# Kernel tuning notes

Hardware: AMD Instinct MI355X
Metric: run time of the kernel (lower is better)

The kernel has to match this reference:

```python
import jax, jax.numpy as jnp
import numpy as np

B, N, R, S, G = 16, 10000, 10, 1000, 4
DIN, DH = 32, 64
DBLK = DIN + DH  # block input dim = input_dim + rnn_units
BIAS_W = jnp.array([0.1, 0.1, 0.1, 1.0], dtype=jnp.float32)


def _block(h, A, rs, W, a1w, a1b, a2w, a2b):
    # h: [B,N,din], A: [G,R,S,S] (shared across batch), rs: [B,N,2]
    Bb, Nn, din = h.shape
    hr = h.reshape(Bb, R, S, din)
    deg = jnp.clip(A.sum(-1), 1e-5) ** -0.5                     # [G,R,S]
    eye = jnp.eye(S, dtype=A.dtype)
    An = deg[..., :, None] * (A + eye) * deg[..., None, :]      # sym-normalized A+I
    hw = jnp.einsum('brsd,gde->gbrse', hr, W)                   # [G,B,R,S,DH]
    outs = jax.nn.relu(jnp.einsum('grst,gbrte->gbrse', An, hw)).reshape(G, Bb, Nn, DH)
    H = jnp.moveaxis(outs, 0, -2).reshape(Bb, Nn, G * DH)       # cat over graphs
    z = jax.nn.relu(jnp.concatenate([H, rs], -1) @ a1w + a1b)
    alpha = jax.nn.softmax(z @ a2w + a2b, axis=-1)              # [B,N,G]
    bias = (rs[:, :, 1] > 0.5).astype(h.dtype)[..., None] * BIAS_W
    alpha = alpha * (1.0 + bias)
    alpha = alpha / alpha.sum(-1, keepdims=True)
    return jnp.einsum('bng,gbne->bne', alpha, outs)


def setup_inputs() -> dict:
    key = jax.random.key(0)
    ks = jax.random.split(key, 16)
    inp = {
        'x_t': jax.random.normal(ks[0], (B, N, DIN), jnp.float32),
        'h_prev': jax.random.normal(ks[1], (B, N, DH), jnp.float32),
        'A': jax.random.uniform(ks[2], (G, R, S, S), jnp.float32),
        'resid_stats': jax.random.uniform(ks[3], (B, N, 2), jnp.float32),
    }
    i = 4
    for tag in ('u', 'r', 'c'):
        inp['W_' + tag] = jax.random.normal(ks[i], (G, DBLK, DH), jnp.float32) * 0.05; i += 1
        inp['a1w_' + tag] = jax.random.normal(ks[i], (G * DH + 2, DH), jnp.float32) * 0.05; i += 1
        inp['a1b_' + tag] = jnp.zeros((DH,), jnp.float32)
        inp['a2w_' + tag] = jax.random.normal(ks[i], (DH, G), jnp.float32) * 0.05; i += 1
        inp['a2b_' + tag] = jnp.zeros((G,), jnp.float32)
    return inp


def reference(x_t, h_prev, A, resid_stats,
              W_u, a1w_u, a1b_u, a2w_u, a2b_u,
              W_r, a1w_r, a1b_r, a2w_r, a2b_r,
              W_c, a1w_c, a1b_c, a2w_c, a2b_c):
    inp = jnp.concatenate([x_t, h_prev], -1)
    U = _block(inp, A, resid_stats, W_u, a1w_u, a1b_u, a2w_u, a2b_u)
    Rg = _block(inp, A, resid_stats, W_r, a1w_r, a1b_r, a2w_r, a2b_r)
    cand = jnp.concatenate([x_t, Rg * h_prev], -1)
    Ht = _block(cand, A, resid_stats, W_c, a1w_c, a1b_c, a2w_c, a2b_c)
    u = jax.nn.sigmoid(U)
    return u * jnp.tanh(Ht) + (1.0 - u) * h_prev
```

## Files before the change

### kernel.cpp

```cpp
#include <hip/hip_runtime.h>

typedef unsigned short u16;
typedef __attribute__((ext_vector_type(8))) short bfrag8;
typedef __attribute__((ext_vector_type(4))) float fvec4;
typedef __attribute__((ext_vector_type(4))) unsigned short usvec4;

#define Bc   16
#define Nn   10000
#define Rr   10
#define Ss   1000
#define Gg   4
#define SP   1024
#define NPAD 10048

__device__ __forceinline__ float bf2f(u16 u) {
  union { unsigned int i; float f; } x; x.i = ((unsigned int)u) << 16; return x.f;
}
__device__ __forceinline__ u16 f2bf(float f) {
  unsigned int x = __float_as_uint(f);
  unsigned int r = x + 0x7FFFu + ((x >> 16) & 1u);
  return (u16)(r >> 16);
}

__global__ __launch_bounds__(256) void prep_weights_kernel(
    const float* __restrict__ Wu, const float* __restrict__ Wr, const float* __restrict__ Wc,
    const float* __restrict__ a1u, const float* __restrict__ a1r, const float* __restrict__ a1c,
    u16* __restrict__ Wt, u16* __restrict__ a1wb)
{
  int idx = blockIdx.x * 256 + threadIdx.x;
  if (idx < 73728) {
    int p = idx / 24576, rem = idx % 24576;
    int g = rem / 6144, r2 = rem % 6144;
    int e = r2 / 96, dd = r2 % 96;
    const float* W = (p == 0) ? Wu : (p == 1) ? Wr : Wc;
    Wt[idx] = f2bf(W[(g * 96 + dd) * 64 + e]);
  } else if (idx < 73728 + 49536) {
    int j = idx - 73728;
    int p = j / 16512, k = j % 16512;
    const float* s = (p == 0) ? a1u : (p == 1) ? a1r : a1c;
    a1wb[j] = f2bf(s[k]);
  }
}

__global__ __launch_bounds__(256) void rowsum_kernel(const float* __restrict__ A,
                                                     float* __restrict__ dis)
{
  int wid = threadIdx.x >> 6, lane = threadIdx.x & 63;
  int row = blockIdx.x * 4 + wid;
  const float* ap = A + (size_t)row * 1000;
  float s = 0.f;
  for (int i = lane; i < 250; i += 64) {
    float4 v = *(const float4*)(ap + i * 4);
    s += (v.x + v.y) + (v.z + v.w);
  }
  #pragma unroll
  for (int off = 32; off >= 1; off >>= 1) s += __shfl_xor(s, off);
  if (lane == 0) dis[row] = rsqrtf(fmaxf(s, 1e-5f));
}

__global__ __launch_bounds__(256) void build_an_kernel(const float* __restrict__ A,
                                                       const float* __restrict__ dis,
                                                       u16* __restrict__ An)
{
  int rowid = blockIdx.x;
  int gr = rowid / 1000, s = rowid % 1000;
  float ds = dis[rowid];
  const float* ap = A + (size_t)rowid * 1000;
  u16* anp = An + (size_t)rowid * SP;
  int t4 = threadIdx.x * 4;
  if (t4 < 1000) {
    float4 a4 = *(const float4*)(ap + t4);
    float4 d4 = *(const float4*)(dis + gr * 1000 + t4);
    float v0 = ds * d4.x * (a4.x + ((t4 + 0) == s ? 1.f : 0.f));
    float v1 = ds * d4.y * (a4.y + ((t4 + 1) == s ? 1.f : 0.f));
    float v2 = ds * d4.z * (a4.z + ((t4 + 2) == s ? 1.f : 0.f));
    float v3 = ds * d4.w * (a4.w + ((t4 + 3) == s ? 1.f : 0.f));
    usvec4 o = {f2bf(v0), f2bf(v1), f2bf(v2), f2bf(v3)};
    *(usvec4*)(anp + t4) = o;
  } else {
    usvec4 o = {0, 0, 0, 0};
    *(usvec4*)(anp + t4) = o;
  }
}

__global__ __launch_bounds__(256) void prep_inpT_kernel(const float* __restrict__ x_t,
                                                        const float* __restrict__ h_prev,
                                                        u16* __restrict__ inpT)
{
  int b = blockIdx.y, n0 = blockIdx.x * 64;
  __shared__ float t[64][97];
  for (int idx = threadIdx.x; idx < 2048; idx += 256) {
    int ni = idx >> 5, d = idx & 31;
    int n = n0 + ni;
    t[ni][d] = (n < Nn) ? x_t[(size_t)(b * Nn + n) * 32 + d] : 0.f;
  }
  for (int idx = threadIdx.x; idx < 4096; idx += 256) {
    int ni = idx >> 6, d = idx & 63;
    int n = n0 + ni;
    t[ni][32 + d] = (n < Nn) ? h_prev[(size_t)(b * Nn + n) * 64 + d] : 0.f;
  }
  __syncthreads();
  for (int idx = threadIdx.x; idx < 6144; idx += 256) {
    int d = idx >> 6, ni = idx & 63;
    inpT[(size_t)b * (96 * NPAD) + (size_t)d * NPAD + n0 + ni] = f2bf(t[ni][d]);
  }
}

template <int NPROJ>
__global__ __launch_bounds__(256) void gemm_pass_kernel(
    const u16* __restrict__ An,
    const u16* __restrict__ inpT,
    const u16* __restrict__ Wt,
    u16* __restrict__ outs0, u16* __restrict__ outs1)
{
  constexpr int BT_OFF = 128 * 40;
  __shared__ __align__(16) u16 lds_main[12288];

  const int tid = threadIdx.x;
  const int lane = tid & 63, wid = tid >> 6;
  const int mt = blockIdx.x, b = blockIdx.y, gr = blockIdx.z;
  const int g = gr / Rr, r = gr % Rr;
  const int m0 = mt * 128;
  const int wrow0 = wid * 32;
  const int lr = lane & 15, lk = (lane >> 4) << 3;

  const u16* Ap = An + (size_t)gr * (Ss * SP);
  const u16* Bp = inpT + (size_t)b * (96 * NPAD) + r * Ss;

  fvec4 acc[2][6];
  #pragma unroll
  for (int i = 0; i < 2; ++i)
    #pragma unroll
    for (int j = 0; j < 6; ++j) acc[i][j] = (fvec4){0.f, 0.f, 0.f, 0.f};

  #pragma unroll 1
  for (int kk = 0; kk < SP; kk += 32) {
    __syncthreads();
    #pragma unroll
    for (int s2 = 0; s2 < 2; ++s2) {
      int seg = tid + (s2 << 8);
      int row = seg >> 2, kl = (seg & 3) << 3;
      int srow = m0 + row;
      bfrag8 v = (bfrag8){0, 0, 0, 0, 0, 0, 0, 0};
      if (srow < Ss) v = *(const bfrag8*)(Ap + (size_t)srow * SP + kk + kl);
      *(bfrag8*)&lds_main[row * 40 + kl] = v;
    }
    {
      int d = tid >> 2, tl = (tid & 3) << 3;
      *(bfrag8*)&lds_main[BT_OFF + d * 40 + tl] = *(const bfrag8*)(Bp + (size_t)d * NPAD + kk + tl);
      if (tid < 128) {
        int seg = 256 + tid;
        int d2 = seg >> 2, t2 = (seg & 3) << 3;
        *(bfrag8*)&lds_main[BT_OFF + d2 * 40 + t2] = *(const bfrag8*)(Bp + (size_t)d2 * NPAD + kk + t2);
      }
    }
    __syncthreads();
    bfrag8 af0 = *(const bfrag8*)&lds_main[(wrow0 + lr) * 40 + lk];
    bfrag8 af1 = *(const bfrag8*)&lds_main[(wrow0 + 16 + lr) * 40 + lk];
    #pragma unroll
    for (int nf = 0; nf < 6; ++nf) {
      bfrag8 bfr = *(const bfrag8*)&lds_main[BT_OFF + (nf * 16 + lr) * 40 + lk];
      acc[0][nf] = __builtin_amdgcn_mfma_f32_16x16x32_bf16(af0, bfr, acc[0][nf], 0, 0, 0);
      acc[1][nf] = __builtin_amdgcn_mfma_f32_16x16x32_bf16(af1, bfr, acc[1][nf], 0, 0, 0);
    }
  }

  __syncthreads();
  #pragma unroll
  for (int mf = 0; mf < 2; ++mf)
    #pragma unroll
    for (int nf = 0; nf < 6; ++nf)
      #pragma unroll
      for (int j = 0; j < 4; ++j) {
        int row = wrow0 + mf * 16 + ((lane >> 4) << 2) + j;
        lds_main[row * 96 + nf * 16 + lr] = f2bf(acc[mf][nf][j]);
      }
  __syncthreads();

  const int obase = ((g * Bc + b) * Nn + r * Ss) * 64;
  #pragma unroll
  for (int p = 0; p < NPROJ; ++p) {
    const u16* Wg = Wt + (size_t)(p * Gg + g) * 6144;
    fvec4 acc2[2][4];
    #pragma unroll
    for (int i = 0; i < 2; ++i)
      #pragma unroll
      for (int j = 0; j < 4; ++j) acc2[i][j] = (fvec4){0.f, 0.f, 0.f, 0.f};
    #pragma unroll
    for (int dk = 0; dk < 96; dk += 32) {
      bfrag8 x0 = *(const bfrag8*)&lds_main[(wrow0 + lr) * 96 + dk + lk];
      bfrag8 x1 = *(const bfrag8*)&lds_main[(wrow0 + 16 + lr) * 96 + dk + lk];
      #pragma unroll
      for (int ef = 0; ef < 4; ++ef) {
        bfrag8 wv = *(const bfrag8*)&Wg[(ef * 16 + lr) * 96 + dk + lk];
        acc2[0][ef] = __builtin_amdgcn_mfma_f32_16x16x32_bf16(x0, wv, acc2[0][ef], 0, 0, 0);
        acc2[1][ef] = __builtin_amdgcn_mfma_f32_16x16x32_bf16(x1, wv, acc2[1][ef], 0, 0, 0);
      }
    }
    u16* op = (p == 0) ? outs0 : outs1;
    #pragma unroll
    for (int mf = 0; mf < 2; ++mf)
      #pragma unroll
      for (int ef = 0; ef < 4; ++ef)
        #pragma unroll
        for (int j = 0; j < 4; ++j) {
          int srow = m0 + wrow0 + mf * 16 + ((lane >> 4) << 2) + j;
          if (srow < Ss) {
            float v = fmaxf(acc2[mf][ef][j], 0.f);
            op[obase + srow * 64 + ef * 16 + lr] = f2bf(v);
          }
        }
  }
}

template <int MODE>
__global__ __launch_bounds__(256) void attn_kernel(
    const u16* __restrict__ outs,
    const float* __restrict__ rs,
    const u16* __restrict__ a1wb,
    const float* __restrict__ a1b, const float* __restrict__ a2w, const float* __restrict__ a2b,
    const float* __restrict__ h_prev, const float* __restrict__ u_sig_in,
    float* __restrict__ usig_out, u16* __restrict__ candh_out, float* __restrict__ out_final)
{
  __shared__ __align__(16) u16 a1wT[16384];
  __shared__ __align__(16) u16 Hs[16384];
  __shared__ __align__(16) float alpha_s[256];

  const int tid = threadIdx.x, lane = tid & 63, w = tid >> 6;
  const int lr16 = lane & 15, hi4 = lane >> 4;
  const int lk = hi4 << 3;
  const int w16 = w * 16;

  {
    int e = tid & 63, kb = (tid >> 6) * 64;
    for (int i = 0; i < 64; ++i) {
      int k = kb + i;
      a1wT[(e * 256 + k) ^ ((e & 7) << 3)] = a1wb[k * 64 + e];
    }
  }

  float a1b_v[4], w256v[4], w257v[4], a2w_l[16], a2b_v[4];
  #pragma unroll
  for (int ef = 0; ef < 4; ++ef) {
    int e = ef * 16 + lr16;
    a1b_v[ef] = a1b[e];
    w256v[ef] = bf2f(a1wb[256 * 64 + e]);
    w257v[ef] = bf2f(a1wb[257 * 64 + e]);
    #pragma unroll
    for (int g = 0; g < 4; ++g) a2w_l[ef * 4 + g] = a2w[e * 4 + g];
  }
  #pragma unroll
  for (int g = 0; g < 4; ++g) a2b_v[g] = a2b[g];

  for (int it = 0; it < 5; ++it) {
    const int row0 = (blockIdx.x * 5 + it) * 64;
    __syncthreads();
    #pragma unroll
    for (int j = 0; j < 8; ++j) {
      int c = tid + j * 256;
      int g = c >> 9, rem = c & 511, ri = rem >> 3, e8 = rem & 7;
      bfrag8 v = *(const bfrag8*)&outs[((size_t)g * (Bc * Nn) + row0 + ri) * 64 + e8 * 8];
      *(bfrag8*)&Hs[(ri * 256 + g * 64 + e8 * 8) ^ ((ri & 7) << 3)] = v;
    }
    __syncthreads();

    fvec4 zacc[4];
    #pragma unroll
    for (int ef = 0; ef < 4; ++ef) zacc[ef] = (fvec4){0.f, 0.f, 0.f, 0.f};
    #pragma unroll
    for (int ks = 0; ks < 8; ++ks) {
      bfrag8 af = *(const bfrag8*)&Hs[((w16 + lr16) * 256 + ks * 32 + lk) ^ ((lr16 & 7) << 3)];
      #pragma unroll
      for (int ef = 0; ef < 4; ++ef) {
        bfrag8 bf = *(const bfrag8*)&a1wT[((ef * 16 + lr16) * 256 + ks * 32 + lk) ^ ((lr16 & 7) << 3)];
        zacc[ef] = __builtin_amdgcn_mfma_f32_16x16x32_bf16(af, bf, zacc[ef], 0, 0, 0);
      }
    }

    float r0[4], r1[4];
    #pragma unroll
    for (int j = 0; j < 4; ++j) {
      int rrow = row0 + w16 + hi4 * 4 + j;
      float2 rv = *(const float2*)(rs + (size_t)rrow * 2);
      r0[j] = rv.x; r1[j] = rv.y;
    }
    float pj[16];
    #pragma unroll
    for (int i = 0; i < 16; ++i) pj[i] = 0.f;
    #pragma unroll
    for (int ef = 0; ef < 4; ++ef)
      #pragma unroll
      for (int j = 0; j < 4; ++j) {
        float zv = zacc[ef][j] + a1b_v[ef] + r0[j] * w256v[ef] + r1[j] * w257v[ef];
        zv = fmaxf(zv, 0.f);
        #pragma unroll
        for (int g = 0; g < 4; ++g) pj[j * 4 + g] = fmaf(zv, a2w_l[ef * 4 + g], pj[j * 4 + g]);
      }
    #pragma unroll
    for (int off = 1; off <= 8; off <<= 1)
      #pragma unroll
      for (int i = 0; i < 16; ++i) pj[i] += __shfl_xor(pj[i], off);

    #pragma unroll
    for (int j = 0; j < 4; ++j) {
      float p0 = pj[j * 4 + 0] + a2b_v[0], p1 = pj[j * 4 + 1] + a2b_v[1];
      float p2 = pj[j * 4 + 2] + a2b_v[2], p3 = pj[j * 4 + 3] + a2b_v[3];
      float m = fmaxf(fmaxf(p0, p1), fmaxf(p2, p3));
      float e0 = __expf(p0 - m), e1 = __expf(p1 - m), e2 = __expf(p2 - m), e3 = __expf(p3 - m);
      if (r1[j] > 0.5f) { e0 *= 1.1f; e1 *= 1.1f; e2 *= 1.1f; e3 *= 2.0f; }
      float inv = 1.f / (e0 + e1 + e2 + e3);
      if (lr16 < 4) {
        float esel = (lr16 == 0) ? e0 : (lr16 == 1) ? e1 : (lr16 == 2) ? e2 : e3;
        alpha_s[(w16 + hi4 * 4 + j) * 4 + lr16] = esel * inv;
      }
    }

    #pragma unroll 1
    for (int rr = 0; rr < 16; ++rr) {
      int lrow = w16 + rr;
      float4 av = *(const float4*)&alpha_s[lrow * 4];
      int sw = (lrow & 7) << 3, base = lrow * 256;
      float cmb = av.x * bf2f(Hs[(base + lane) ^ sw])
                + av.y * bf2f(Hs[(base + 64 + lane) ^ sw])
                + av.z * bf2f(Hs[(base + 128 + lane) ^ sw])
                + av.w * bf2f(Hs[(base + 192 + lane) ^ sw]);
      size_t gi = (size_t)(row0 + lrow) * 64 + lane;
      if (MODE == 0) {
        usig_out[gi] = 1.f / (1.f + __expf(-cmb));
      } else if (MODE == 1) {
        candh_out[gi] = f2bf(cmb * h_prev[gi]);
      } else {
        float u = u_sig_in[gi], hp = h_prev[gi];
        out_final[gi] = u * tanhf(cmb) + (1.f - u) * hp;
      }
    }
  }
}

__global__ __launch_bounds__(256) void transpose_cand_kernel(const u16* __restrict__ candh,
                                                             u16* __restrict__ inpT)
{
  int b = blockIdx.y, n0 = blockIdx.x * 64;
  __shared__ float t[64][65];
  for (int idx = threadIdx.x; idx < 4096; idx += 256) {
    int ni = idx >> 6, e = idx & 63;
    int n = n0 + ni;
    t[ni][e] = (n < Nn) ? bf2f(candh[(size_t)(b * Nn + n) * 64 + e]) : 0.f;
  }
  __syncthreads();
  for (int idx = threadIdx.x; idx < 4096; idx += 256) {
    int e = idx >> 6, ni = idx & 63;
    inpT[(size_t)b * (96 * NPAD) + (size_t)(32 + e) * NPAD + n0 + ni] = f2bf(t[ni][e]);
  }
}

extern "C" void kernel_launch(void* const* d_in, const int* in_sizes, int n_in,
                              void* d_out, int out_size, void* d_ws, size_t ws_size,
                              hipStream_t stream) {
  (void)in_sizes; (void)n_in; (void)out_size; (void)ws_size;
  const float* x_t    = (const float*)d_in[0];
  const float* h_prev = (const float*)d_in[1];
  const float* A      = (const float*)d_in[2];
  const float* rs     = (const float*)d_in[3];
  const float* W_u    = (const float*)d_in[4];
  const float* a1w_u  = (const float*)d_in[5];
  const float* a1b_u  = (const float*)d_in[6];
  const float* a2w_u  = (const float*)d_in[7];
  const float* a2b_u  = (const float*)d_in[8];
  const float* W_r    = (const float*)d_in[9];
  const float* a1w_r  = (const float*)d_in[10];
  const float* a1b_r  = (const float*)d_in[11];
  const float* a2w_r  = (const float*)d_in[12];
  const float* a2b_r  = (const float*)d_in[13];
  const float* W_c    = (const float*)d_in[14];
  const float* a1w_c  = (const float*)d_in[15];
  const float* a1b_c  = (const float*)d_in[16];
  const float* a2w_c  = (const float*)d_in[17];
  const float* a2b_c  = (const float*)d_in[18];
  float* out = (float*)d_out;

  char* ws = (char*)d_ws;
  const size_t AN_OFF    = 0;
  const size_t DIS_OFF   = 81920000;
  const size_t INPT_OFF  = 82080000;
  const size_t OUTSU_OFF = 112947456;
  const size_t OUTSR_OFF = 194867456;
  const size_t USIG_OFF  = 276787456;
  const size_t CANDH_OFF = 317747456;
  const size_t WT_OFF    = 338227456;
  const size_t A1WB_OFF  = 338374912;

  u16* An    = (u16*)(ws + AN_OFF);
  float* dis = (float*)(ws + DIS_OFF);
  u16* inpT  = (u16*)(ws + INPT_OFF);
  u16* outsU = (u16*)(ws + OUTSU_OFF);
  u16* outsR = (u16*)(ws + OUTSR_OFF);
  u16* outsC = outsU;
  float* usig = (float*)(ws + USIG_OFF);
  u16* candh = (u16*)(ws + CANDH_OFF);
  u16* Wt    = (u16*)(ws + WT_OFF);
  u16* a1wb  = (u16*)(ws + A1WB_OFF);

  prep_weights_kernel<<<482, 256, 0, stream>>>(W_u, W_r, W_c, a1w_u, a1w_r, a1w_c, Wt, a1wb);
  rowsum_kernel<<<10000, 256, 0, stream>>>(A, dis);
  build_an_kernel<<<40000, 256, 0, stream>>>(A, dis, An);
  prep_inpT_kernel<<<dim3(157, 16), 256, 0, stream>>>(x_t, h_prev, inpT);

  gemm_pass_kernel<2><<<dim3(8, 16, 40), 256, 0, stream>>>(An, inpT, Wt, outsU, outsR);

  attn_kernel<0><<<500, 256, 0, stream>>>(outsU, rs, a1wb, a1b_u, a2w_u, a2b_u,
                                          nullptr, nullptr, usig, nullptr, nullptr);
  attn_kernel<1><<<500, 256, 0, stream>>>(outsR, rs, a1wb + 16512, a1b_r, a2w_r, a2b_r,
                                          h_prev, nullptr, nullptr, candh, nullptr);
  transpose_cand_kernel<<<dim3(157, 16), 256, 0, stream>>>(candh, inpT);

  gemm_pass_kernel<1><<<dim3(8, 16, 40), 256, 0, stream>>>(An, inpT, Wt + 2 * 24576, outsC, nullptr);

  attn_kernel<2><<<500, 256, 0, stream>>>(outsC, rs, a1wb + 2 * 16512, a1b_c, a2w_c, a2b_c,
                                          h_prev, usig, nullptr, nullptr, out);
}
```

Before: 1.156 ms.

## Restructure GRU graph GEMMs with direct-to-LDS loads and reordered candidate projection

Replaces the A-hat x input GEMM with a version that stages tiles via global_load_lds into XOR-swizzled LDS with 64-wide K steps and a 2x2 wave layout. The candidate block now projects through W first (cand_proj_kernel) and then multiplies by An with a wider N tile. That removes the 96-dim input GEMM and the separate transpose kernel. The attention kernels take a pre-transposed a1w from global memory instead of rebuilding it in LDS, run one tile per block across more blocks, and store usig as bf16. An is padded to 1024 rows so loads need no bounds checks. The costs are extra workspace layout changes and somewhat more bf16 rounding.

```diff
diff --git a/kernel.cpp b/kernel.cpp
--- a/kernel.cpp
+++ b/kernel.cpp
@@ -11,6 +11,7 @@
 #define Ss   1000
 #define Gg   4
 #define SP   1024
+#define MP   1024
 #define NPAD 10048
 
 __device__ __forceinline__ float bf2f(u16 u) {
@@ -22,10 +23,28 @@
   return (u16)(r >> 16);
 }
 
+__device__ __forceinline__ void glds16(const u16* gsrc, u16* ldst) {
+  __builtin_amdgcn_global_load_lds((const __attribute__((address_space(1))) unsigned int*)gsrc,
+                                   (__attribute__((address_space(3))) unsigned int*)ldst, 16, 0, 0);
+}
+
+__device__ __forceinline__ void stage_tile(const u16* gsrc, size_t rstride, int nloads,
+                                           u16* ldsbase, int wid, int lane) {
+  int rsub = lane >> 3;
+  int kb8 = ((lane & 7) ^ rsub) << 3;
+  for (int i = wid; i < nloads; i += 4)
+    glds16(gsrc + (size_t)(8 * i + rsub) * rstride + kb8, ldsbase + i * 512);
+}
+
+__device__ __forceinline__ bfrag8 ldsw(const u16* base, int row, int kbyte) {
+  int off = row * 128 + (kbyte ^ ((row & 7) << 4));
+  return *(const bfrag8*)((const char*)base + off);
+}
+
 __global__ __launch_bounds__(256) void prep_weights_kernel(
     const float* __restrict__ Wu, const float* __restrict__ Wr, const float* __restrict__ Wc,
     const float* __restrict__ a1u, const float* __restrict__ a1r, const float* __restrict__ a1c,
-    u16* __restrict__ Wt, u16* __restrict__ a1wb)
+    u16* __restrict__ Wt, u16* __restrict__ a1wb, u16* __restrict__ a1wT)
 {
   int idx = blockIdx.x * 256 + threadIdx.x;
   if (idx < 73728) {
@@ -39,6 +58,12 @@
     int p = j / 16512, k = j % 16512;
     const float* s = (p == 0) ? a1u : (p == 1) ? a1r : a1c;
     a1wb[j] = f2bf(s[k]);
+  } else if (idx < 73728 + 49536 + 49152) {
+    int j = idx - 123264;
+    int p = j / 16384, rem = j % 16384;
+    int e = rem / 256, k = rem % 256;
+    const float* s = (p == 0) ? a1u : (p == 1) ? a1r : a1c;
+    a1wT[j] = f2bf(s[k * 64 + e]);
   }
 }
 
@@ -62,30 +87,31 @@
                                                        const float* __restrict__ dis,
                                                        u16* __restrict__ An)
 {
-  int rowid = blockIdx.x;
-  int gr = rowid / 1000, s = rowid % 1000;
+  int gr = blockIdx.x >> 10, s = blockIdx.x & 1023;
+  u16* anp = An + (size_t)blockIdx.x * 1024;
+  int t4 = threadIdx.x * 4;
+  if (s >= Ss || t4 >= 1000) {
+    usvec4 z = {0, 0, 0, 0};
+    *(usvec4*)(anp + t4) = z;
+    return;
+  }
+  int rowid = gr * 1000 + s;
   float ds = dis[rowid];
   const float* ap = A + (size_t)rowid * 1000;
-  u16* anp = An + (size_t)rowid * SP;
-  int t4 = threadIdx.x * 4;
-  if (t4 < 1000) {
-    float4 a4 = *(const float4*)(ap + t4);
-    float4 d4 = *(const float4*)(dis + gr * 1000 + t4);
-    float v0 = ds * d4.x * (a4.x + ((t4 + 0) == s ? 1.f : 0.f));
-    float v1 = ds * d4.y * (a4.y + ((t4 + 1) == s ? 1.f : 0.f));
-    float v2 = ds * d4.z * (a4.z + ((t4 + 2) == s ? 1.f : 0.f));
-    float v3 = ds * d4.w * (a4.w + ((t4 + 3) == s ? 1.f : 0.f));
-    usvec4 o = {f2bf(v0), f2bf(v1), f2bf(v2), f2bf(v3)};
-    *(usvec4*)(anp + t4) = o;
-  } else {
-    usvec4 o = {0, 0, 0, 0};
-    *(usvec4*)(anp + t4) = o;
-  }
+  float4 a4 = *(const float4*)(ap + t4);
+  float4 d4 = *(const float4*)(dis + gr * 1000 + t4);
+  float v0 = ds * d4.x * (a4.x + ((t4 + 0) == s ? 1.f : 0.f));
+  float v1 = ds * d4.y * (a4.y + ((t4 + 1) == s ? 1.f : 0.f));
+  float v2 = ds * d4.z * (a4.z + ((t4 + 2) == s ? 1.f : 0.f));
+  float v3 = ds * d4.w * (a4.w + ((t4 + 3) == s ? 1.f : 0.f));
+  usvec4 o = {f2bf(v0), f2bf(v1), f2bf(v2), f2bf(v3)};
+  *(usvec4*)(anp + t4) = o;
 }
 
 __global__ __launch_bounds__(256) void prep_inpT_kernel(const float* __restrict__ x_t,
                                                         const float* __restrict__ h_prev,
-                                                        u16* __restrict__ inpT)
+                                                        u16* __restrict__ inpT,
+                                                        u16* __restrict__ candb)
 {
   int b = blockIdx.y, n0 = blockIdx.x * 64;
   __shared__ float t[64][97];
@@ -104,82 +130,77 @@
     int d = idx >> 6, ni = idx & 63;
     inpT[(size_t)b * (96 * NPAD) + (size_t)d * NPAD + n0 + ni] = f2bf(t[ni][d]);
   }
-}
-
-template <int NPROJ>
-__global__ __launch_bounds__(256) void gemm_pass_kernel(
+  for (int idx = threadIdx.x; idx < 2048; idx += 256) {
+    int ni = idx >> 5, d = idx & 31;
+    int n = n0 + ni;
+    if (n < Nn) candb[((size_t)b * Nn + n) * 96 + d] = f2bf(t[ni][d]);
+  }
+}
+
+__global__ __launch_bounds__(256) void gemm_uv_kernel(
     const u16* __restrict__ An,
     const u16* __restrict__ inpT,
     const u16* __restrict__ Wt,
     u16* __restrict__ outs0, u16* __restrict__ outs1)
 {
-  constexpr int BT_OFF = 128 * 40;
-  __shared__ __align__(16) u16 lds_main[12288];
-
-  const int tid = threadIdx.x;
-  const int lane = tid & 63, wid = tid >> 6;
+  __shared__ __align__(1024) u16 lds[14336];
+
+  const int tid = threadIdx.x, lane = tid & 63, wid = tid >> 6;
   const int mt = blockIdx.x, b = blockIdx.y, gr = blockIdx.z;
   const int g = gr / Rr, r = gr % Rr;
   const int m0 = mt * 128;
-  const int wrow0 = wid * 32;
-  const int lr = lane & 15, lk = (lane >> 4) << 3;
-
-  const u16* Ap = An + (size_t)gr * (Ss * SP);
+  const int wrow0 = (wid >> 1) * 64, wcol0 = (wid & 1) * 48;
+  const int lr = lane & 15, hi = lane >> 4;
+  const int kbhi = hi * 16;
+
+  const u16* Ap = An + (size_t)gr * (MP * SP) + (size_t)m0 * SP;
   const u16* Bp = inpT + (size_t)b * (96 * NPAD) + r * Ss;
 
-  fvec4 acc[2][6];
-  #pragma unroll
-  for (int i = 0; i < 2; ++i)
-    #pragma unroll
-    for (int j = 0; j < 6; ++j) acc[i][j] = (fvec4){0.f, 0.f, 0.f, 0.f};
+  fvec4 acc[4][3];
+  #pragma unroll
+  for (int i = 0; i < 4; ++i)
+    #pragma unroll
+    for (int j = 0; j < 3; ++j) acc[i][j] = (fvec4){0.f, 0.f, 0.f, 0.f};
 
   #pragma unroll 1
-  for (int kk = 0; kk < SP; kk += 32) {
+  for (int kt = 0; kt < 16; ++kt) {
+    const int kk = kt * 64;
     __syncthreads();
-    #pragma unroll
-    for (int s2 = 0; s2 < 2; ++s2) {
-      int seg = tid + (s2 << 8);
-      int row = seg >> 2, kl = (seg & 3) << 3;
-      int srow = m0 + row;
-      bfrag8 v = (bfrag8){0, 0, 0, 0, 0, 0, 0, 0};
-      if (srow < Ss) v = *(const bfrag8*)(Ap + (size_t)srow * SP + kk + kl);
-      *(bfrag8*)&lds_main[row * 40 + kl] = v;
-    }
-    {
-      int d = tid >> 2, tl = (tid & 3) << 3;
-      *(bfrag8*)&lds_main[BT_OFF + d * 40 + tl] = *(const bfrag8*)(Bp + (size_t)d * NPAD + kk + tl);
-      if (tid < 128) {
-        int seg = 256 + tid;
-        int d2 = seg >> 2, t2 = (seg & 3) << 3;
-        *(bfrag8*)&lds_main[BT_OFF + d2 * 40 + t2] = *(const bfrag8*)(Bp + (size_t)d2 * NPAD + kk + t2);
-      }
-    }
+    stage_tile(Ap + kk, SP, 16, lds, wid, lane);
+    stage_tile(Bp + kk, NPAD, 12, lds + 8192, wid, lane);
     __syncthreads();
-    bfrag8 af0 = *(const bfrag8*)&lds_main[(wrow0 + lr) * 40 + lk];
-    bfrag8 af1 = *(const bfrag8*)&lds_main[(wrow0 + 16 + lr) * 40 + lk];
-    #pragma unroll
-    for (int nf = 0; nf < 6; ++nf) {
-      bfrag8 bfr = *(const bfrag8*)&lds_main[BT_OFF + (nf * 16 + lr) * 40 + lk];
-      acc[0][nf] = __builtin_amdgcn_mfma_f32_16x16x32_bf16(af0, bfr, acc[0][nf], 0, 0, 0);
-      acc[1][nf] = __builtin_amdgcn_mfma_f32_16x16x32_bf16(af1, bfr, acc[1][nf], 0, 0, 0);
+    #pragma unroll
+    for (int ks = 0; ks < 2; ++ks) {
+      bfrag8 a[4], bb[3];
+      #pragma unroll
+      for (int mfi = 0; mfi < 4; ++mfi) a[mfi] = ldsw(lds, wrow0 + mfi * 16 + lr, ks * 64 + kbhi);
+      #pragma unroll
+      for (int nfi = 0; nfi < 3; ++nfi) bb[nfi] = ldsw(lds + 8192, wcol0 + nfi * 16 + lr, ks * 64 + kbhi);
+      #pragma unroll
+      for (int mfi = 0; mfi < 4; ++mfi)
+        #pragma unroll
+        for (int nfi = 0; nfi < 3; ++nfi)
+          acc[mfi][nfi] = __builtin_amdgcn_mfma_f32_16x16x32_bf16(a[mfi], bb[nfi], acc[mfi][nfi], 0, 0, 0);
     }
   }
 
   __syncthreads();
   #pragma unroll
-  for (int mf = 0; mf < 2; ++mf)
-    #pragma unroll
-    for (int nf = 0; nf < 6; ++nf)
+  for (int mfi = 0; mfi < 4; ++mfi)
+    #pragma unroll
+    for (int nfi = 0; nfi < 3; ++nfi)
       #pragma unroll
       for (int j = 0; j < 4; ++j) {
-        int row = wrow0 + mf * 16 + ((lane >> 4) << 2) + j;
-        lds_main[row * 96 + nf * 16 + lr] = f2bf(acc[mf][nf][j]);
+        int row = wrow0 + mfi * 16 + hi * 4 + j;
+        int col = wcol0 + nfi * 16 + lr;
+        lds[row * 104 + col] = f2bf(acc[mfi][nfi][j]);
       }
   __syncthreads();
 
+  const int s2r0 = wid * 32;
   const int obase = ((g * Bc + b) * Nn + r * Ss) * 64;
   #pragma unroll
-  for (int p = 0; p < NPROJ; ++p) {
+  for (int p = 0; p < 2; ++p) {
     const u16* Wg = Wt + (size_t)(p * Gg + g) * 6144;
     fvec4 acc2[2][4];
     #pragma unroll
@@ -187,12 +208,12 @@
       #pragma unroll
       for (int j = 0; j < 4; ++j) acc2[i][j] = (fvec4){0.f, 0.f, 0.f, 0.f};
     #pragma unroll
-    for (int dk = 0; dk < 96; dk += 32) {
-      bfrag8 x0 = *(const bfrag8*)&lds_main[(wrow0 + lr) * 96 + dk + lk];
-      bfrag8 x1 = *(const bfrag8*)&lds_main[(wrow0 + 16 + lr) * 96 + dk + lk];
+    for (int dk = 0; dk < 3; ++dk) {
+      bfrag8 x0 = *(const bfrag8*)&lds[(s2r0 + lr) * 104 + dk * 32 + kbhi / 2];
+      bfrag8 x1 = *(const bfrag8*)&lds[(s2r0 + 16 + lr) * 104 + dk * 32 + kbhi / 2];
       #pragma unroll
       for (int ef = 0; ef < 4; ++ef) {
-        bfrag8 wv = *(const bfrag8*)&Wg[(ef * 16 + lr) * 96 + dk + lk];
+        bfrag8 wv = *(const bfrag8*)&Wg[(ef * 16 + lr) * 96 + dk * 32 + kbhi / 2];
         acc2[0][ef] = __builtin_amdgcn_mfma_f32_16x16x32_bf16(x0, wv, acc2[0][ef], 0, 0, 0);
         acc2[1][ef] = __builtin_amdgcn_mfma_f32_16x16x32_bf16(x1, wv, acc2[1][ef], 0, 0, 0);
       }
@@ -204,7 +225,7 @@
       for (int ef = 0; ef < 4; ++ef)
         #pragma unroll
         for (int j = 0; j < 4; ++j) {
-          int srow = m0 + wrow0 + mf * 16 + ((lane >> 4) << 2) + j;
+          int srow = m0 + s2r0 + mf * 16 + hi * 4 + j;
           if (srow < Ss) {
             float v = fmaxf(acc2[mf][ef][j], 0.f);
             op[obase + srow * 64 + ef * 16 + lr] = f2bf(v);
@@ -213,16 +234,128 @@
   }
 }
 
+__global__ __launch_bounds__(256) void cand_proj_kernel(const u16* __restrict__ candb,
+                                                        const u16* __restrict__ Wt,
+                                                        u16* __restrict__ hwcT)
+{
+  __shared__ __align__(16) u16 lds[16384];
+  const int tid = threadIdx.x, lane = tid & 63, g = tid >> 6;
+  const int lr = lane & 15, hi = lane >> 4;
+  const int b = blockIdx.y, n0 = blockIdx.x * 64;
+  const u16* WcT = Wt + (size_t)(2 * Gg + g) * 6144;
+
+  fvec4 acc[4][4];
+  #pragma unroll
+  for (int i = 0; i < 4; ++i)
+    #pragma unroll
+    for (int j = 0; j < 4; ++j) acc[i][j] = (fvec4){0.f, 0.f, 0.f, 0.f};
+
+  #pragma unroll
+  for (int ks = 0; ks < 3; ++ks) {
+    bfrag8 a[4], w[4];
+    #pragma unroll
+    for (int mfi = 0; mfi < 4; ++mfi)
+      a[mfi] = *(const bfrag8*)&candb[((size_t)b * Nn + n0 + mfi * 16 + lr) * 96 + ks * 32 + hi * 8];
+    #pragma unroll
+    for (int nfi = 0; nfi < 4; ++nfi)
+      w[nfi] = *(const bfrag8*)&WcT[(nfi * 16 + lr) * 96 + ks * 32 + hi * 8];
+    #pragma unroll
+    for (int mfi = 0; mfi < 4; ++mfi)
+      #pragma unroll
+      for (int nfi = 0; nfi < 4; ++nfi)
+        acc[mfi][nfi] = __builtin_amdgcn_mfma_f32_16x16x32_bf16(a[mfi], w[nfi], acc[mfi][nfi], 0, 0, 0);
+  }
+
+  #pragma unroll
+  for (int mfi = 0; mfi < 4; ++mfi)
+    #pragma unroll
+    for (int nfi = 0; nfi < 4; ++nfi)
+      #pragma unroll
+      for (int j = 0; j < 4; ++j) {
+        int e = nfi * 16 + lr, tl = mfi * 16 + hi * 4 + j;
+        lds[g * 4096 + e * 64 + tl] = f2bf(acc[mfi][nfi][j]);
+      }
+  __syncthreads();
+  #pragma unroll
+  for (int i = 0; i < 8; ++i) {
+    int e = i * 8 + (lane >> 3), tc = lane & 7;
+    bfrag8 v = *(const bfrag8*)&lds[g * 4096 + e * 64 + tc * 8];
+    *(bfrag8*)&hwcT[((size_t)g * 1024 + b * 64 + e) * NPAD + n0 + tc * 8] = v;
+  }
+}
+
+__global__ __launch_bounds__(256) void gemm_c_kernel(
+    const u16* __restrict__ An,
+    const u16* __restrict__ hwcT,
+    u16* __restrict__ outs0)
+{
+  __shared__ __align__(1024) u16 lds[16384];
+
+  const int tid = threadIdx.x, lane = tid & 63, wid = tid >> 6;
+  const int mt = blockIdx.x, by = blockIdx.y, gr = blockIdx.z;
+  const int g = gr / Rr, r = gr % Rr;
+  const int m0 = mt * 128;
+  const int wrow0 = (wid >> 1) * 64, wcol0 = (wid & 1) * 64;
+  const int lr = lane & 15, hi = lane >> 4;
+  const int kbhi = hi * 16;
+
+  const u16* Ap = An + (size_t)gr * (MP * SP) + (size_t)m0 * SP;
+  const u16* Bp = hwcT + (size_t)(g * 1024 + by * 128) * NPAD + r * Ss;
+
+  fvec4 acc[4][4];
+  #pragma unroll
+  for (int i = 0; i < 4; ++i)
+    #pragma unroll
+    for (int j = 0; j < 4; ++j) acc[i][j] = (fvec4){0.f, 0.f, 0.f, 0.f};
+
+  #pragma unroll 1
+  for (int kt = 0; kt < 16; ++kt) {
+    const int kk = kt * 64;
+    __syncthreads();
+    stage_tile(Ap + kk, SP, 16, lds, wid, lane);
+    stage_tile(Bp + kk, NPAD, 16, lds + 8192, wid, lane);
+    __syncthreads();
+    #pragma unroll
+    for (int ks = 0; ks < 2; ++ks) {
+      bfrag8 a[4], bb[4];
+      #pragma unroll
+      for (int mfi = 0; mfi < 4; ++mfi) a[mfi] = ldsw(lds, wrow0 + mfi * 16 + lr, ks * 64 + kbhi);
+      #pragma unroll
+      for (int nfi = 0; nfi < 4; ++nfi) bb[nfi] = ldsw(lds + 8192, wcol0 + nfi * 16 + lr, ks * 64 + kbhi);
+      #pragma unroll
+      for (int mfi = 0; mfi < 4; ++mfi)
+        #pragma unroll
+        for (int nfi = 0; nfi < 4; ++nfi)
+          acc[mfi][nfi] = __builtin_amdgcn_mfma_f32_16x16x32_bf16(a[mfi], bb[nfi], acc[mfi][nfi], 0, 0, 0);
+    }
+  }
+
+  #pragma unroll
+  for (int mfi = 0; mfi < 4; ++mfi)
+    #pragma unroll
+    for (int nfi = 0; nfi < 4; ++nfi)
+      #pragma unroll
+      for (int j = 0; j < 4; ++j) {
+        int srow = m0 + wrow0 + mfi * 16 + hi * 4 + j;
+        if (srow < Ss) {
+          int col = wcol0 + nfi * 16 + lr;
+          int bb2 = by * 2 + (col >> 6), e = col & 63;
+          int n = r * Ss + srow;
+          outs0[(((size_t)g * Bc + bb2) * Nn + n) * 64 + e] = f2bf(fmaxf(acc[mfi][nfi][j], 0.f));
+        }
+      }
+}
+
 template <int MODE>
 __global__ __launch_bounds__(256) void attn_kernel(
     const u16* __restrict__ outs,
     const float* __restrict__ rs,
+    const u16* __restrict__ a1wT,
     const u16* __restrict__ a1wb,
     const float* __restrict__ a1b, const float* __restrict__ a2w, const float* __restrict__ a2b,
-    const float* __restrict__ h_prev, const float* __restrict__ u_sig_in,
-    float* __restrict__ usig_out, u16* __restrict__ candh_out, float* __restrict__ out_final)
-{
-  __shared__ __align__(16) u16 a1wT[16384];
+    const float* __restrict__ h_prev, const u16* __restrict__ usig_in,
+    u16* __restrict__ usig_out, u16* __restrict__ candb_out, float* __restrict__ out_final)
+{
   __shared__ __align__(16) u16 Hs[16384];
   __shared__ __align__(16) float alpha_s[256];
 
@@ -230,13 +363,14 @@
   const int lr16 = lane & 15, hi4 = lane >> 4;
   const int lk = hi4 << 3;
   const int w16 = w * 16;
-
-  {
-    int e = tid & 63, kb = (tid >> 6) * 64;
-    for (int i = 0; i < 64; ++i) {
-      int k = kb + i;
-      a1wT[(e * 256 + k) ^ ((e & 7) << 3)] = a1wb[k * 64 + e];
-    }
+  const int row0 = blockIdx.x * 64;
+
+  #pragma unroll
+  for (int j = 0; j < 8; ++j) {
+    int c = tid + j * 256;
+    int g = c >> 9, rem = c & 511, ri = rem >> 3, e8 = rem & 7;
+    bfrag8 v = *(const bfrag8*)&outs[((size_t)g * (Bc * Nn) + row0 + ri) * 64 + e8 * 8];
+    *(bfrag8*)&Hs[(ri * 256 + g * 64 + e8 * 8) ^ ((ri & 7) << 3)] = v;
   }
 
   float a1b_v[4], w256v[4], w257v[4], a2w_l[16], a2b_v[4];
@@ -251,106 +385,78 @@
   }
   #pragma unroll
   for (int g = 0; g < 4; ++g) a2b_v[g] = a2b[g];
-
-  for (int it = 0; it < 5; ++it) {
-    const int row0 = (blockIdx.x * 5 + it) * 64;
-    __syncthreads();
-    #pragma unroll
-    for (int j = 0; j < 8; ++j) {
-      int c = tid + j * 256;
-      int g = c >> 9, rem = c & 511, ri = rem >> 3, e8 = rem & 7;
-      bfrag8 v = *(const bfrag8*)&outs[((size_t)g * (Bc * Nn) + row0 + ri) * 64 + e8 * 8];
-      *(bfrag8*)&Hs[(ri * 256 + g * 64 + e8 * 8) ^ ((ri & 7) << 3)] = v;
-    }
-    __syncthreads();
-
-    fvec4 zacc[4];
-    #pragma unroll
-    for (int ef = 0; ef < 4; ++ef) zacc[ef] = (fvec4){0.f, 0.f, 0.f, 0.f};
-    #pragma unroll
-    for (int ks = 0; ks < 8; ++ks) {
-      bfrag8 af = *(const bfrag8*)&Hs[((w16 + lr16) * 256 + ks * 32 + lk) ^ ((lr16 & 7) << 3)];
-      #pragma unroll
-      for (int ef = 0; ef < 4; ++ef) {
-        bfrag8 bf = *(const bfrag8*)&a1wT[((ef * 16 + lr16) * 256 + ks * 32 + lk) ^ ((lr16 & 7) << 3)];
-        zacc[ef] = __builtin_amdgcn_mfma_f32_16x16x32_bf16(af, bf, zacc[ef], 0, 0, 0);
-      }
-    }
-
-    float r0[4], r1[4];
+  __syncthreads();
+
+  fvec4 zacc[4];
+  #pragma unroll
+  for (int ef = 0; ef < 4; ++ef) zacc[ef] = (fvec4){0.f, 0.f, 0.f, 0.f};
+  #pragma unroll
+  for (int ks = 0; ks < 8; ++ks) {
+    bfrag8 af = *(const bfrag8*)&Hs[((w16 + lr16) * 256 + ks * 32 + lk) ^ ((lr16 & 7) << 3)];
+    #pragma unroll
+    for (int ef = 0; ef < 4; ++ef) {
+      bfrag8 bf = *(const bfrag8*)&a1wT[(ef * 16 + lr16) * 256 + ks * 32 + lk];
+      zacc[ef] = __builtin_amdgcn_mfma_f32_16x16x32_bf16(af, bf, zacc[ef], 0, 0, 0);
+    }
+  }
+
+  float r0[4], r1[4];
+  #pragma unroll
+  for (int j = 0; j < 4; ++j) {
+    int rrow = row0 + w16 + hi4 * 4 + j;
+    float2 rv = *(const float2*)(rs + (size_t)rrow * 2);
+    r0[j] = rv.x; r1[j] = rv.y;
+  }
+  float pj[16];
+  #pragma unroll
+  for (int i = 0; i < 16; ++i) pj[i] = 0.f;
+  #pragma unroll
+  for (int ef = 0; ef < 4; ++ef)
     #pragma unroll
     for (int j = 0; j < 4; ++j) {
-      int rrow = row0 + w16 + hi4 * 4 + j;
-      float2 rv = *(const float2*)(rs + (size_t)rrow * 2);
-      r0[j] = rv.x; r1[j] = rv.y;
-    }
-    float pj[16];
-    #pragma unroll
-    for (int i = 0; i < 16; ++i) pj[i] = 0.f;
-    #pragma unroll
-    for (int ef = 0; ef < 4; ++ef)
-      #pragma unroll
-      for (int j = 0; j < 4; ++j) {
-        float zv = zacc[ef][j] + a1b_v[ef] + r0[j] * w256v[ef] + r1[j] * w257v[ef];
-        zv = fmaxf(zv, 0.f);
-        #pragma unroll
-        for (int g = 0; g < 4; ++g) pj[j * 4 + g] = fmaf(zv, a2w_l[ef * 4 + g], pj[j * 4 + g]);
-      }
-    #pragma unroll
-    for (int off = 1; off <= 8; off <<= 1)
-      #pragma unroll
-      for (int i = 0; i < 16; ++i) pj[i] += __shfl_xor(pj[i], off);
-
-    #pragma unroll
-    for (int j = 0; j < 4; ++j) {
-      float p0 = pj[j * 4 + 0] + a2b_v[0], p1 = pj[j * 4 + 1] + a2b_v[1];
-      float p2 = pj[j * 4 + 2] + a2b_v[2], p3 = pj[j * 4 + 3] + a2b_v[3];
-      float m = fmaxf(fmaxf(p0, p1), fmaxf(p2, p3));
-      float e0 = __expf(p0 - m), e1 = __expf(p1 - m), e2 = __expf(p2 - m), e3 = __expf(p3 - m);
-      if (r1[j] > 0.5f) { e0 *= 1.1f; e1 *= 1.1f; e2 *= 1.1f; e3 *= 2.0f; }
-      float inv = 1.f / (e0 + e1 + e2 + e3);
-      if (lr16 < 4) {
-        float esel = (lr16 == 0) ? e0 : (lr16 == 1) ? e1 : (lr16 == 2) ? e2 : e3;
-        alpha_s[(w16 + hi4 * 4 + j) * 4 + lr16] = esel * inv;
-      }
-    }
-
-    #pragma unroll 1
-    for (int rr = 0; rr < 16; ++rr) {
-      int lrow = w16 + rr;
-      float4 av = *(const float4*)&alpha_s[lrow * 4];
-      int sw = (lrow & 7) << 3, base = lrow * 256;
-      float cmb = av.x * bf2f(Hs[(base + lane) ^ sw])
-                + av.y * bf2f(Hs[(base + 64 + lane) ^ sw])
-                + av.z * bf2f(Hs[(base + 128 + lane) ^ sw])
-                + av.w * bf2f(Hs[(base + 192 + lane) ^ sw]);
-      size_t gi = (size_t)(row0 + lrow) * 64 + lane;
-      if (MODE == 0) {
-        usig_out[gi] = 1.f / (1.f + __expf(-cmb));
-      } else if (MODE == 1) {
-        candh_out[gi] = f2bf(cmb * h_prev[gi]);
-      } else {
-        float u = u_sig_in[gi], hp = h_prev[gi];
-        out_final[gi] = u * tanhf(cmb) + (1.f - u) * hp;
-      }
-    }
-  }
-}
-
-__global__ __launch_bounds__(256) void transpose_cand_kernel(const u16* __restrict__ candh,
-                                                             u16* __restrict__ inpT)
-{
-  int b = blockIdx.y, n0 = blockIdx.x * 64;
-  __shared__ float t[64][65];
-  for (int idx = threadIdx.x; idx < 4096; idx += 256) {
-    int ni = idx >> 6, e = idx & 63;
-    int n = n0 + ni;
-    t[ni][e] = (n < Nn) ? bf2f(candh[(size_t)(b * Nn + n) * 64 + e]) : 0.f;
-  }
-  __syncthreads();
-  for (int idx = threadIdx.x; idx < 4096; idx += 256) {
-    int e = idx >> 6, ni = idx & 63;
-    inpT[(size_t)b * (96 * NPAD) + (size_t)(32 + e) * NPAD + n0 + ni] = f2bf(t[ni][e]);
+      float zv = zacc[ef][j] + a1b_v[ef] + r0[j] * w256v[ef] + r1[j] * w257v[ef];
+      zv = fmaxf(zv, 0.f);
+      #pragma unroll
+      for (int g = 0; g < 4; ++g) pj[j * 4 + g] = fmaf(zv, a2w_l[ef * 4 + g], pj[j * 4 + g]);
+    }
+  #pragma unroll
+  for (int off = 1; off <= 8; off <<= 1)
+    #pragma unroll
+    for (int i = 0; i < 16; ++i) pj[i] += __shfl_xor(pj[i], off);
+
+  #pragma unroll
+  for (int j = 0; j < 4; ++j) {
+    float p0 = pj[j * 4 + 0] + a2b_v[0], p1 = pj[j * 4 + 1] + a2b_v[1];
+    float p2 = pj[j * 4 + 2] + a2b_v[2], p3 = pj[j * 4 + 3] + a2b_v[3];
+    float m = fmaxf(fmaxf(p0, p1), fmaxf(p2, p3));
+    float e0 = __expf(p0 - m), e1 = __expf(p1 - m), e2 = __expf(p2 - m), e3 = __expf(p3 - m);
+    if (r1[j] > 0.5f) { e0 *= 1.1f; e1 *= 1.1f; e2 *= 1.1f; e3 *= 2.0f; }
+    float inv = 1.f / (e0 + e1 + e2 + e3);
+    if (lr16 < 4) {
+      float esel = (lr16 == 0) ? e0 : (lr16 == 1) ? e1 : (lr16 == 2) ? e2 : e3;
+      alpha_s[(w16 + hi4 * 4 + j) * 4 + lr16] = esel * inv;
+    }
+  }
+
+  #pragma unroll 1
+  for (int rr = 0; rr < 16; ++rr) {
+    int lrow = w16 + rr;
+    float4 av = *(const float4*)&alpha_s[lrow * 4];
+    int sw = (lrow & 7) << 3, base = lrow * 256;
+    float cmb = av.x * bf2f(Hs[(base + lane) ^ sw])
+              + av.y * bf2f(Hs[(base + 64 + lane) ^ sw])
+              + av.z * bf2f(Hs[(base + 128 + lane) ^ sw])
+              + av.w * bf2f(Hs[(base + 192 + lane) ^ sw]);
+    size_t row = (size_t)(row0 + lrow);
+    size_t gi = row * 64 + lane;
+    if (MODE == 0) {
+      usig_out[gi] = f2bf(1.f / (1.f + __expf(-cmb)));
+    } else if (MODE == 1) {
+      candb_out[row * 96 + 32 + lane] = f2bf(cmb * h_prev[gi]);
+    } else {
+      float u = bf2f(usig_in[gi]), hp = h_prev[gi];
+      out_final[gi] = u * tanhf(cmb) + (1.f - u) * hp;
+    }
   }
 }
 
@@ -381,41 +487,44 @@
 
   char* ws = (char*)d_ws;
   const size_t AN_OFF    = 0;
-  const size_t DIS_OFF   = 81920000;
-  const size_t INPT_OFF  = 82080000;
-  const size_t OUTSU_OFF = 112947456;
-  const size_t OUTSR_OFF = 194867456;
-  const size_t USIG_OFF  = 276787456;
-  const size_t CANDH_OFF = 317747456;
-  const size_t WT_OFF    = 338227456;
-  const size_t A1WB_OFF  = 338374912;
+  const size_t DIS_OFF   = 83886080;
+  const size_t INPT_OFF  = 84046080;
+  const size_t OUTSU_OFF = 114913536;
+  const size_t OUTSR_OFF = 196833536;
+  const size_t USIG_OFF  = 279146752;
+  const size_t CANDB_OFF = 299626752;
+  const size_t WT_OFF    = 330346752;
+  const size_t A1WB_OFF  = 330494208;
+  const size_t A1WT_OFF  = 330593280;
 
   u16* An    = (u16*)(ws + AN_OFF);
   float* dis = (float*)(ws + DIS_OFF);
   u16* inpT  = (u16*)(ws + INPT_OFF);
   u16* outsU = (u16*)(ws + OUTSU_OFF);
   u16* outsR = (u16*)(ws + OUTSR_OFF);
+  u16* hwcT  = (u16*)(ws + OUTSR_OFF);
   u16* outsC = outsU;
-  float* usig = (float*)(ws + USIG_OFF);
-  u16* candh = (u16*)(ws + CANDH_OFF);
+  u16* usig  = (u16*)(ws + USIG_OFF);
+  u16* candb = (u16*)(ws + CANDB_OFF);
   u16* Wt    = (u16*)(ws + WT_OFF);
   u16* a1wb  = (u16*)(ws + A1WB_OFF);
-
-  prep_weights_kernel<<<482, 256, 0, stream>>>(W_u, W_r, W_c, a1w_u, a1w_r, a1w_c, Wt, a1wb);
+  u16* a1wT  = (u16*)(ws + A1WT_OFF);
+
+  prep_weights_kernel<<<674, 256, 0, stream>>>(W_u, W_r, W_c, a1w_u, a1w_r, a1w_c, Wt, a1wb, a1wT);
   rowsum_kernel<<<10000, 256, 0, stream>>>(A, dis);
-  build_an_kernel<<<40000, 256, 0, stream>>>(A, dis, An);
-  prep_inpT_kernel<<<dim3(157, 16), 256, 0, stream>>>(x_t, h_prev, inpT);
-
-  gemm_pass_kernel<2><<<dim3(8, 16, 40), 256, 0, stream>>>(An, inpT, Wt, outsU, outsR);
-
-  attn_kernel<0><<<500, 256, 0, stream>>>(outsU, rs, a1wb, a1b_u, a2w_u, a2b_u,
-                                          nullptr, nullptr, usig, nullptr, nullptr);
-  attn_kernel<1><<<500, 256, 0, stream>>>(outsR, rs, a1wb + 16512, a1b_r, a2w_r, a2b_r,
-                                          h_prev, nullptr, nullptr, candh, nullptr);
-  transpose_cand_kernel<<<dim3(157, 16), 256, 0, stream>>>(candh, inpT);
-
-  gemm_pass_kernel<1><<<dim3(8, 16, 40), 256, 0, stream>>>(An, inpT, Wt + 2 * 24576, outsC, nullptr);
-
-  attn_kernel<2><<<500, 256, 0, stream>>>(outsC, rs, a1wb + 2 * 16512, a1b_c, a2w_c, a2b_c,
-                                          h_prev, usig, nullptr, nullptr, out);
-}
+  build_an_kernel<<<40960, 256, 0, stream>>>(A, dis, An);
+  prep_inpT_kernel<<<dim3(157, 16), 256, 0, stream>>>(x_t, h_prev, inpT, candb);
+
+  gemm_uv_kernel<<<dim3(8, 16, 40), 256, 0, stream>>>(An, inpT, Wt, outsU, outsR);
+
+  attn_kernel<0><<<2500, 256, 0, stream>>>(outsU, rs, a1wT, a1wb, a1b_u, a2w_u, a2b_u,
+                                           nullptr, nullptr, usig, nullptr, nullptr);
+  attn_kernel<1><<<2500, 256, 0, stream>>>(outsR, rs, a1wT + 16384, a1wb + 16512, a1b_r, a2w_r, a2b_r,
+                                           h_prev, nullptr, nullptr, candb, nullptr);
+
+  cand_proj_kernel<<<dim3(157, 16), 256, 0, stream>>>(candb, Wt, hwcT);
+  gemm_c_kernel<<<dim3(8, 8, 40), 256, 0, stream>>>(An, hwcT, outsC);
+
+  attn_kernel<2><<<2500, 256, 0, stream>>>(outsC, rs, a1wT + 32768, a1wb + 33024, a1b_c, a2w_c, a2b_c,
+                                           h_prev, usig, nullptr, nullptr, out);
+}
```

Result: faster. 956.7 us (-17.2%).
